# Kernel optimization log

Measured on AMD Instinct MI355X. Metric: run time of the kernel, lower is better.

## Reference

```python
import jax, jax.numpy as jnp
import numpy as np

EPS = 1e-5  # torch LayerNorm default

def _ln(x, w, b):
    mu = jnp.mean(x, axis=-1, keepdims=True)
    var = jnp.mean((x - mu) ** 2, axis=-1, keepdims=True)
    return (x - mu) * jax.lax.rsqrt(var + EPS) * w + b

def setup_inputs() -> dict:
    B, C, P, D = 256, 256, 256, 256  # broadcasting in final add requires B==P==C
    key = jax.random.key(0)
    ks = jax.random.split(key, 10)
    d_rsqrt = D ** -0.5
    return {
        "x": jax.random.normal(ks[0], (B, C), dtype=jnp.float32),
        "prev_cell_out": jax.random.normal(ks[1], (P, D), dtype=jnp.float32),
        "feature_emb_weight": jax.random.uniform(ks[2], (C, D), minval=-d_rsqrt, maxval=d_rsqrt),
        "feature_emb_bias": jax.random.uniform(ks[3], (1, C, D), minval=-d_rsqrt, maxval=d_rsqrt),
        "ln_emb_w": jnp.ones((D,), jnp.float32), "ln_emb_b": jnp.zeros((D,), jnp.float32),
        "ln_col_w": jnp.ones((D,), jnp.float32), "ln_col_b": jnp.zeros((D,), jnp.float32),
        "ln_prompt_w": jnp.ones((D,), jnp.float32), "ln_prompt_b": jnp.zeros((D,), jnp.float32),
        "dense_imp_w": jax.random.normal(ks[4], (D, 2 * D)) * (2 * D) ** -0.5,  # torch Linear weight [out,in]
        "dense_imp_b": jnp.zeros((D,), jnp.float32),
        "emb_column": jax.random.normal(ks[5], (C, D)) * 0.01,
        "emb_prompt": jax.random.normal(ks[6], (P, D)) * 0.01,
        "expand_weight": jax.random.normal(ks[7], (P, 1)),  # dense_expand.weight [n_prompts, 1]
        "expand_bias": jax.random.normal(ks[8], (P,)) * 0.01,
    }

def reference(x, prev_cell_out, feature_emb_weight, feature_emb_bias,
              ln_emb_w, ln_emb_b, ln_col_w, ln_col_b, ln_prompt_w, ln_prompt_b,
              dense_imp_w, dense_imp_b, emb_column, emb_prompt,
              expand_weight, expand_bias):
    # addcmul: bias + x[...,None] * weight -> [B, C, D]
    x_emb = _ln(jax.nn.relu(feature_emb_bias + x[..., None] * feature_emb_weight), ln_emb_w, ln_emb_b)
    # prompt path (unbatched): [P, 2D] -> [P, D]
    xp_in = jnp.concatenate([_ln(emb_prompt, ln_prompt_w, ln_prompt_b), prev_cell_out], axis=-1)
    x_prompt = xp_in @ dense_imp_w.T + dense_imp_b + emb_prompt
    x_col = _ln(emb_column, ln_col_w, ln_col_b)  # [C, D]
    mask = jax.nn.softmax(x_prompt @ x_col.T, axis=-1)  # [P, C]
    # einsum 'pc,bcd->bpd'
    x_out = jnp.einsum('pc,bcd->bpd', mask, x_emb)
    # 'pc,bcd,pa->bpd' with a==1 is the same contraction scaled per-prompt by expand_weight[p,0]
    x_out = x_out * (1.0 + expand_weight[:, 0])[None, :, None]
    # 'pc,p->pc' then unsqueeze(0).unsqueeze(-1): [1, P, C, 1]; broadcasts [B,P,D] -> [1,B,P,D]
    bias_term = (mask * expand_bias[:, None])[None, :, :, None]
    return x_out + bias_term  # [1, B, P, D] (B==P==C)
```

## Files before the change

### kernel.cpp

```cpp
#include <hip/hip_runtime.h>
#include <cstdint>

typedef _Float16 half8 __attribute__((ext_vector_type(8)));
typedef float f32x4 __attribute__((ext_vector_type(4)));

#define LN_EPS 1e-5f

__device__ __forceinline__ void gl2lds16(const void* g, void* l) {
  __builtin_amdgcn_global_load_lds((const __attribute__((address_space(1))) uint32_t*)g,
                                   (__attribute__((address_space(3))) uint32_t*)l, 16, 0, 0);
}

__global__ __launch_bounds__(256) void k_ln_rows(
    const float* __restrict__ emb_prompt, const float* __restrict__ lnp_w, const float* __restrict__ lnp_b,
    const float* __restrict__ emb_column, const float* __restrict__ lnc_w, const float* __restrict__ lnc_b,
    float* __restrict__ out_prompt, float* __restrict__ out_col)
{
  int row = blockIdx.x * 4 + (threadIdx.x >> 6);
  int lane = threadIdx.x & 63;
  const float *src, *wp, *bp; float* dst; int r;
  if (row < 256) { src = emb_prompt; wp = lnp_w; bp = lnp_b; dst = out_prompt; r = row; }
  else           { src = emb_column; wp = lnc_w; bp = lnc_b; dst = out_col;    r = row - 256; }
  float4 v = ((const float4*)src)[r * 64 + lane];
  float s1 = v.x + v.y + v.z + v.w;
  float s2 = v.x*v.x + v.y*v.y + v.z*v.z + v.w*v.w;
  #pragma unroll
  for (int o = 32; o > 0; o >>= 1) { s1 += __shfl_xor(s1, o); s2 += __shfl_xor(s2, o); }
  float mu  = s1 * (1.0f/256.0f);
  float var = s2 * (1.0f/256.0f) - mu*mu;
  float rs  = rsqrtf(var + LN_EPS);
  float4 w4 = ((const float4*)wp)[lane];
  float4 b4 = ((const float4*)bp)[lane];
  float4 y;
  y.x = (v.x-mu)*rs*w4.x + b4.x;
  y.y = (v.y-mu)*rs*w4.y + b4.y;
  y.z = (v.z-mu)*rs*w4.z + b4.z;
  y.w = (v.w-mu)*rs*w4.w + b4.w;
  ((float4*)dst)[r * 64 + lane] = y;
}

__global__ __launch_bounds__(256) void k_xprompt(
    const float* __restrict__ ln_prompt, const float* __restrict__ prev,
    const float* __restrict__ W, const float* __restrict__ bias,
    const float* __restrict__ emb_prompt, float* __restrict__ xprompt)
{
  __shared__ float xp[4][512];
  int t = threadIdx.x;
  int pb = blockIdx.x * 4;
  #pragma unroll
  for (int r = 0; r < 4; ++r) {
    xp[r][t]       = ln_prompt[(pb+r)*256 + t];
    xp[r][256 + t] = prev[(pb+r)*256 + t];
  }
  __syncthreads();
  float acc[4] = {0.f, 0.f, 0.f, 0.f};
  const float4* W4 = (const float4*)(W + (size_t)t * 512);
  for (int k4 = 0; k4 < 128; ++k4) {
    float4 wv = W4[k4];
    #pragma unroll
    for (int r = 0; r < 4; ++r) {
      float4 xq = ((const float4*)xp[r])[k4];
      acc[r] += wv.x*xq.x + wv.y*xq.y + wv.z*xq.z + wv.w*xq.w;
    }
  }
  float bb = bias[t];
  #pragma unroll
  for (int r = 0; r < 4; ++r)
    xprompt[(pb+r)*256 + t] = acc[r] + bb + emb_prompt[(pb+r)*256 + t];
}

__global__ __launch_bounds__(256) void k_mask(
    const float* __restrict__ xprompt, const float* __restrict__ xcol,
    float* __restrict__ mask_f32, _Float16* __restrict__ mask_f16)
{
  __shared__ float xp[4][256];
  __shared__ float4 wred[4];
  __shared__ float4 wred2[4];
  int t = threadIdx.x, w = t >> 6, lane = t & 63;
  int pb = blockIdx.x * 4;
  #pragma unroll
  for (int r = 0; r < 4; ++r) xp[r][t] = xprompt[(pb+r)*256 + t];
  __syncthreads();
  float sc[4] = {0.f, 0.f, 0.f, 0.f};
  const float4* c4 = (const float4*)(xcol + (size_t)t * 256);
  for (int d4 = 0; d4 < 64; ++d4) {
    float4 cv = c4[d4];
    #pragma unroll
    for (int r = 0; r < 4; ++r) {
      float4 xq = ((const float4*)xp[r])[d4];
      sc[r] += cv.x*xq.x + cv.y*xq.y + cv.z*xq.z + cv.w*xq.w;
    }
  }
  float m[4] = {sc[0], sc[1], sc[2], sc[3]};
  #pragma unroll
  for (int o = 32; o > 0; o >>= 1) {
    #pragma unroll
    for (int r = 0; r < 4; ++r) m[r] = fmaxf(m[r], __shfl_xor(m[r], o));
  }
  if (lane == 0) wred[w] = make_float4(m[0], m[1], m[2], m[3]);
  __syncthreads();
  float4 a0 = wred[0], a1 = wred[1], a2 = wred[2], a3 = wred[3];
  float M[4] = { fmaxf(fmaxf(a0.x,a1.x), fmaxf(a2.x,a3.x)),
                 fmaxf(fmaxf(a0.y,a1.y), fmaxf(a2.y,a3.y)),
                 fmaxf(fmaxf(a0.z,a1.z), fmaxf(a2.z,a3.z)),
                 fmaxf(fmaxf(a0.w,a1.w), fmaxf(a2.w,a3.w)) };
  float e[4], s[4];
  #pragma unroll
  for (int r = 0; r < 4; ++r) { e[r] = expf(sc[r] - M[r]); s[r] = e[r]; }
  #pragma unroll
  for (int o = 32; o > 0; o >>= 1) {
    #pragma unroll
    for (int r = 0; r < 4; ++r) s[r] += __shfl_xor(s[r], o);
  }
  if (lane == 0) wred2[w] = make_float4(s[0], s[1], s[2], s[3]);
  __syncthreads();
  float4 b0 = wred2[0], b1 = wred2[1], b2 = wred2[2], b3 = wred2[3];
  float S[4] = { b0.x+b1.x+b2.x+b3.x, b0.y+b1.y+b2.y+b3.y,
                 b0.z+b1.z+b2.z+b3.z, b0.w+b1.w+b2.w+b3.w };
  #pragma unroll
  for (int r = 0; r < 4; ++r) {
    float mv = e[r] / S[r];
    mask_f32[(pb+r)*256 + t] = mv;
    mask_f16[(pb+r)*256 + t] = (_Float16)mv;
  }
}

__global__ __launch_bounds__(256) void k_xemb(
    const float* __restrict__ x, const float* __restrict__ few, const float* __restrict__ feb,
    const float* __restrict__ lnw, const float* __restrict__ lnb, _Float16* __restrict__ emb)
{
  __shared__ float ldsv[8][256];
  __shared__ float stat_mu[8], stat_rs[8];
  int t = threadIdx.x, w = t >> 6, lane = t & 63;
  int b = blockIdx.x >> 5, cg = blockIdx.x & 31;
  float v[8];
  #pragma unroll
  for (int cl = 0; cl < 8; ++cl) {
    int c = cg*8 + cl;
    float xv = x[b*256 + c];
    float val = feb[c*256 + t] + xv * few[c*256 + t];
    v[cl] = fmaxf(val, 0.f);
    ldsv[cl][t] = v[cl];
  }
  __syncthreads();
  #pragma unroll
  for (int j = 0; j < 2; ++j) {
    int cl = w*2 + j;
    float4 a = ((const float4*)ldsv[cl])[lane];
    float s1 = a.x + a.y + a.z + a.w;
    float s2 = a.x*a.x + a.y*a.y + a.z*a.z + a.w*a.w;
    #pragma unroll
    for (int o = 32; o > 0; o >>= 1) { s1 += __shfl_xor(s1, o); s2 += __shfl_xor(s2, o); }
    if (lane == 0) {
      float mu  = s1 * (1.0f/256.0f);
      float var = s2 * (1.0f/256.0f) - mu*mu;
      stat_mu[cl] = mu;
      stat_rs[cl] = rsqrtf(var + LN_EPS);
    }
  }
  __syncthreads();
  float lw = lnw[t], lb = lnb[t];
  half8 h;
  #pragma unroll
  for (int cl = 0; cl < 8; ++cl)
    h[cl] = (_Float16)((v[cl] - stat_mu[cl]) * stat_rs[cl] * lw + lb);
  ((uint4*)emb)[(size_t)cg*65536 + (size_t)b*256 + t] = *(const uint4*)&h;
}

__global__ __launch_bounds__(256) void k_gemm(
    const _Float16* __restrict__ Bmat,
    const _Float16* __restrict__ Amask,
    const float* __restrict__ mask_f32,
    const float* __restrict__ ew, const float* __restrict__ eb,
    float* __restrict__ out)
{
  __shared__ __align__(16) _Float16 As[128 * 72];
  __shared__ __align__(16) _Float16 Bs[8 * 128 * 8];
  int t = threadIdx.x, w = t >> 6, lane = t & 63;
  int lm = lane & 15, quad = lane >> 4;
  int wm = (w & 1) * 64, wn = (w >> 1) * 64;
  int p0 = blockIdx.x * 128;
  int n0 = blockIdx.y * 128;

  f32x4 acc[4][4];
  #pragma unroll
  for (int i = 0; i < 4; ++i)
    #pragma unroll
    for (int j = 0; j < 4; ++j)
      acc[i][j] = (f32x4){0.f, 0.f, 0.f, 0.f};

  for (int kb = 0; kb < 4; ++kb) {
    int k0 = kb * 64;
    if (kb) __syncthreads();
    #pragma unroll
    for (int i = 0; i < 4; ++i) {
      int u = i*256 + t;
      int chi = u >> 7, np = u & 127;
      gl2lds16(Bmat + (size_t)(kb*8 + chi)*524288 + (size_t)(n0 + np)*8, Bs + (size_t)u*8);
    }
    uint4 av[4];
    #pragma unroll
    for (int i = 0; i < 4; ++i) {
      int u = i*256 + t;
      int m = u >> 3, k8 = u & 7;
      av[i] = *(const uint4*)(Amask + (size_t)(p0 + m)*256 + k0 + k8*8);
    }
    #pragma unroll
    for (int i = 0; i < 4; ++i) {
      int u = i*256 + t;
      int m = u >> 3, k8 = u & 7;
      *(uint4*)(As + m*72 + k8*8) = av[i];
    }
    __syncthreads();
    #pragma unroll
    for (int ks = 0; ks < 2; ++ks) {
      half8 af[4], bf[4];
      #pragma unroll
      for (int mt = 0; mt < 4; ++mt)
        af[mt] = *(const half8*)(As + (wm + mt*16 + lm)*72 + ks*32 + quad*8);
      #pragma unroll
      for (int nt = 0; nt < 4; ++nt)
        bf[nt] = *(const half8*)(Bs + ((ks*4 + quad)*128 + wn + nt*16 + lm)*8);
      #pragma unroll
      for (int mt = 0; mt < 4; ++mt)
        #pragma unroll
        for (int nt = 0; nt < 4; ++nt)
          acc[mt][nt] = __builtin_amdgcn_mfma_f32_16x16x32_f16(af[mt], bf[nt], acc[mt][nt], 0, 0, 0);
    }
  }

  int b = n0 >> 8;
  float ebv = eb[b];
  #pragma unroll
  for (int mt = 0; mt < 4; ++mt) {
    float sp[4], tb[4];
    #pragma unroll
    for (int r = 0; r < 4; ++r) {
      int p = p0 + wm + mt*16 + quad*4 + r;
      sp[r] = 1.0f + ew[p];
      tb[r] = mask_f32[b*256 + p] * ebv;
    }
    #pragma unroll
    for (int nt = 0; nt < 4; ++nt) {
      int d = (n0 & 255) + wn + nt*16 + lm;
      #pragma unroll
      for (int r = 0; r < 4; ++r) {
        int p = p0 + wm + mt*16 + quad*4 + r;
        out[((size_t)b << 16) + ((size_t)p << 8) + d] = acc[mt][nt][r] * sp[r] + tb[r];
      }
    }
  }
}

extern "C" void kernel_launch(void* const* d_in, const int* in_sizes, int n_in,
                              void* d_out, int out_size, void* d_ws, size_t ws_size,
                              hipStream_t stream) {
  const float* x        = (const float*)d_in[0];
  const float* prev     = (const float*)d_in[1];
  const float* few      = (const float*)d_in[2];
  const float* feb      = (const float*)d_in[3];
  const float* ln_emb_w = (const float*)d_in[4];
  const float* ln_emb_b = (const float*)d_in[5];
  const float* ln_col_w = (const float*)d_in[6];
  const float* ln_col_b = (const float*)d_in[7];
  const float* ln_pr_w  = (const float*)d_in[8];
  const float* ln_pr_b  = (const float*)d_in[9];
  const float* dimp_w   = (const float*)d_in[10];
  const float* dimp_b   = (const float*)d_in[11];
  const float* emb_col  = (const float*)d_in[12];
  const float* emb_pr   = (const float*)d_in[13];
  const float* ew       = (const float*)d_in[14];
  const float* eb       = (const float*)d_in[15];
  float* out = (float*)d_out;

  char* wsb = (char*)d_ws;
  _Float16* ws_emb    = (_Float16*)(wsb);
  float*    ws_mask   = (float*)(wsb + 33554432);
  _Float16* ws_mask_h = (_Float16*)(wsb + 33816576);
  float*    ws_lnp    = (float*)(wsb + 33947648);
  float*    ws_xcol   = (float*)(wsb + 34209792);
  float*    ws_xp     = (float*)(wsb + 34471936);

  k_ln_rows<<<dim3(128), dim3(256), 0, stream>>>(emb_pr, ln_pr_w, ln_pr_b,
                                                 emb_col, ln_col_w, ln_col_b,
                                                 ws_lnp, ws_xcol);
  k_xprompt<<<dim3(64), dim3(256), 0, stream>>>(ws_lnp, prev, dimp_w, dimp_b, emb_pr, ws_xp);
  k_mask<<<dim3(64), dim3(256), 0, stream>>>(ws_xp, ws_xcol, ws_mask, ws_mask_h);
  k_xemb<<<dim3(8192), dim3(256), 0, stream>>>(x, few, feb, ln_emb_w, ln_emb_b, ws_emb);
  k_gemm<<<dim3(2, 512), dim3(256), 0, stream>>>(ws_emb, ws_mask_h, ws_mask, ew, eb, out);
}
```

Before: 182.0 us.

## Fuse prompt/mask pipeline and x_emb into one kernel; stream A from global in GEMM

Measured after the change: 243.7 us. 33.9% more time.

```diff
diff --git a/kernel.cpp b/kernel.cpp
--- a/kernel.cpp
+++ b/kernel.cpp
@@ -11,171 +11,220 @@
                                    (__attribute__((address_space(3))) uint32_t*)l, 16, 0, 0);
 }
 
-__global__ __launch_bounds__(256) void k_ln_rows(
-    const float* __restrict__ emb_prompt, const float* __restrict__ lnp_w, const float* __restrict__ lnp_b,
-    const float* __restrict__ emb_column, const float* __restrict__ lnc_w, const float* __restrict__ lnc_b,
-    float* __restrict__ out_prompt, float* __restrict__ out_col)
+__device__ __forceinline__ float dot4(float4 a, float4 b) {
+  return a.x*b.x + a.y*b.y + a.z*b.z + a.w*b.w;
+}
+
+__global__ __launch_bounds__(256) void k_fused(
+    const float* __restrict__ x, const float* __restrict__ few, const float* __restrict__ feb,
+    const float* __restrict__ ln_emb_w, const float* __restrict__ ln_emb_b,
+    const float* __restrict__ emb_pr, const float* __restrict__ lnp_w, const float* __restrict__ lnp_b,
+    const float* __restrict__ prev, const float* __restrict__ W, const float* __restrict__ Wb,
+    const float* __restrict__ emb_col, const float* __restrict__ lnc_w, const float* __restrict__ lnc_b,
+    float* __restrict__ mask_f32, _Float16* __restrict__ mask_f16, _Float16* __restrict__ emb)
 {
-  int row = blockIdx.x * 4 + (threadIdx.x >> 6);
-  int lane = threadIdx.x & 63;
-  const float *src, *wp, *bp; float* dst; int r;
-  if (row < 256) { src = emb_prompt; wp = lnp_w; bp = lnp_b; dst = out_prompt; r = row; }
-  else           { src = emb_column; wp = lnc_w; bp = lnc_b; dst = out_col;    r = row - 256; }
-  float4 v = ((const float4*)src)[r * 64 + lane];
-  float s1 = v.x + v.y + v.z + v.w;
-  float s2 = v.x*v.x + v.y*v.y + v.z*v.z + v.w*v.w;
-  #pragma unroll
-  for (int o = 32; o > 0; o >>= 1) { s1 += __shfl_xor(s1, o); s2 += __shfl_xor(s2, o); }
-  float mu  = s1 * (1.0f/256.0f);
-  float var = s2 * (1.0f/256.0f) - mu*mu;
-  float rs  = rsqrtf(var + LN_EPS);
-  float4 w4 = ((const float4*)wp)[lane];
-  float4 b4 = ((const float4*)bp)[lane];
-  float4 y;
-  y.x = (v.x-mu)*rs*w4.x + b4.x;
-  y.y = (v.y-mu)*rs*w4.y + b4.y;
-  y.z = (v.z-mu)*rs*w4.z + b4.z;
-  y.w = (v.w-mu)*rs*w4.w + b4.w;
-  ((float4*)dst)[r * 64 + lane] = y;
-}
-
-__global__ __launch_bounds__(256) void k_xprompt(
-    const float* __restrict__ ln_prompt, const float* __restrict__ prev,
-    const float* __restrict__ W, const float* __restrict__ bias,
-    const float* __restrict__ emb_prompt, float* __restrict__ xprompt)
-{
-  __shared__ float xp[4][512];
-  int t = threadIdx.x;
-  int pb = blockIdx.x * 4;
-  #pragma unroll
-  for (int r = 0; r < 4; ++r) {
-    xp[r][t]       = ln_prompt[(pb+r)*256 + t];
-    xp[r][256 + t] = prev[(pb+r)*256 + t];
+  __shared__ __align__(16) union SMem {
+    struct {
+      float xin[4][512];
+      float xq[4][256];
+      float cmu[256], crs[256];
+      float sc[4][256];
+      float4 wr1[4], wr2[4];
+    } m;
+    struct {
+      float v[32][256];
+      float mu[32], rs[32];
+    } e;
+  } sm;
+
+  int t = threadIdx.x, w = t >> 6, lane = t & 63;
+
+  if (blockIdx.x < 64) {
+    int pb = blockIdx.x * 4;
+    {
+      int p = pb + w;
+      float4 v = ((const float4*)emb_pr)[p * 64 + lane];
+      float s1 = v.x + v.y + v.z + v.w;
+      float s2 = v.x*v.x + v.y*v.y + v.z*v.z + v.w*v.w;
+      #pragma unroll
+      for (int o = 32; o > 0; o >>= 1) { s1 += __shfl_xor(s1, o); s2 += __shfl_xor(s2, o); }
+      float mu = s1 * (1.0f/256.0f);
+      float var = s2 * (1.0f/256.0f) - mu*mu;
+      float rs = rsqrtf(var + LN_EPS);
+      float4 w4 = ((const float4*)lnp_w)[lane];
+      float4 b4 = ((const float4*)lnp_b)[lane];
+      float4 y;
+      y.x = (v.x-mu)*rs*w4.x + b4.x;  y.y = (v.y-mu)*rs*w4.y + b4.y;
+      y.z = (v.z-mu)*rs*w4.z + b4.z;  y.w = (v.w-mu)*rs*w4.w + b4.w;
+      ((float4*)sm.m.xin[w])[lane] = y;
+      ((float4*)sm.m.xin[w])[64 + lane] = ((const float4*)prev)[p * 64 + lane];
+    }
+    for (int i = 0; i < 64; ++i) {
+      int c = w * 64 + i;
+      float4 v = ((const float4*)emb_col)[c * 64 + lane];
+      float s1 = v.x + v.y + v.z + v.w;
+      float s2 = v.x*v.x + v.y*v.y + v.z*v.z + v.w*v.w;
+      #pragma unroll
+      for (int o = 32; o > 0; o >>= 1) { s1 += __shfl_xor(s1, o); s2 += __shfl_xor(s2, o); }
+      if (lane == 0) {
+        float mu = s1 * (1.0f/256.0f);
+        float var = s2 * (1.0f/256.0f) - mu*mu;
+        sm.m.cmu[c] = mu;
+        sm.m.crs[c] = rsqrtf(var + LN_EPS);
+      }
+    }
+    __syncthreads();
+    {
+      float4 xa[4], xb[4];
+      #pragma unroll
+      for (int r = 0; r < 4; ++r) {
+        xa[r] = ((const float4*)sm.m.xin[r])[lane];
+        xb[r] = ((const float4*)sm.m.xin[r])[64 + lane];
+      }
+      for (int i = 0; i < 64; ++i) {
+        int d = w * 64 + i;
+        float4 wa = ((const float4*)W)[d * 128 + lane];
+        float4 wc = ((const float4*)W)[d * 128 + 64 + lane];
+        float a0 = dot4(wa, xa[0]) + dot4(wc, xb[0]);
+        float a1 = dot4(wa, xa[1]) + dot4(wc, xb[1]);
+        float a2 = dot4(wa, xa[2]) + dot4(wc, xb[2]);
+        float a3 = dot4(wa, xa[3]) + dot4(wc, xb[3]);
+        #pragma unroll
+        for (int o = 32; o > 0; o >>= 1) {
+          a0 += __shfl_xor(a0, o); a1 += __shfl_xor(a1, o);
+          a2 += __shfl_xor(a2, o); a3 += __shfl_xor(a3, o);
+        }
+        if (lane == 0) {
+          float bb = Wb[d];
+          sm.m.xq[0][d] = a0 + bb + emb_pr[(pb+0)*256 + d];
+          sm.m.xq[1][d] = a1 + bb + emb_pr[(pb+1)*256 + d];
+          sm.m.xq[2][d] = a2 + bb + emb_pr[(pb+2)*256 + d];
+          sm.m.xq[3][d] = a3 + bb + emb_pr[(pb+3)*256 + d];
+        }
+      }
+    }
+    __syncthreads();
+    {
+      float4 lw4 = ((const float4*)lnc_w)[lane];
+      float4 lb4 = ((const float4*)lnc_b)[lane];
+      float4 xr[4];
+      #pragma unroll
+      for (int r = 0; r < 4; ++r) xr[r] = ((const float4*)sm.m.xq[r])[lane];
+      for (int i = 0; i < 64; ++i) {
+        int c = w * 64 + i;
+        float4 v = ((const float4*)emb_col)[c * 64 + lane];
+        float mu = sm.m.cmu[c], rs = sm.m.crs[c];
+        float4 nc;
+        nc.x = (v.x-mu)*rs*lw4.x + lb4.x;  nc.y = (v.y-mu)*rs*lw4.y + lb4.y;
+        nc.z = (v.z-mu)*rs*lw4.z + lb4.z;  nc.w = (v.w-mu)*rs*lw4.w + lb4.w;
+        float a0 = dot4(nc, xr[0]), a1 = dot4(nc, xr[1]);
+        float a2 = dot4(nc, xr[2]), a3 = dot4(nc, xr[3]);
+        #pragma unroll
+        for (int o = 32; o > 0; o >>= 1) {
+          a0 += __shfl_xor(a0, o); a1 += __shfl_xor(a1, o);
+          a2 += __shfl_xor(a2, o); a3 += __shfl_xor(a3, o);
+        }
+        if (lane == 0) {
+          sm.m.sc[0][c] = a0; sm.m.sc[1][c] = a1;
+          sm.m.sc[2][c] = a2; sm.m.sc[3][c] = a3;
+        }
+      }
+    }
+    __syncthreads();
+    {
+      float val[4];
+      #pragma unroll
+      for (int r = 0; r < 4; ++r) val[r] = sm.m.sc[r][t];
+      float m0[4] = {val[0], val[1], val[2], val[3]};
+      #pragma unroll
+      for (int o = 32; o > 0; o >>= 1)
+        #pragma unroll
+        for (int r = 0; r < 4; ++r) m0[r] = fmaxf(m0[r], __shfl_xor(m0[r], o));
+      if (lane == 0) sm.m.wr1[w] = make_float4(m0[0], m0[1], m0[2], m0[3]);
+      __syncthreads();
+      float4 a0 = sm.m.wr1[0], a1 = sm.m.wr1[1], a2 = sm.m.wr1[2], a3 = sm.m.wr1[3];
+      float M[4] = { fmaxf(fmaxf(a0.x,a1.x), fmaxf(a2.x,a3.x)),
+                     fmaxf(fmaxf(a0.y,a1.y), fmaxf(a2.y,a3.y)),
+                     fmaxf(fmaxf(a0.z,a1.z), fmaxf(a2.z,a3.z)),
+                     fmaxf(fmaxf(a0.w,a1.w), fmaxf(a2.w,a3.w)) };
+      float e[4], s[4];
+      #pragma unroll
+      for (int r = 0; r < 4; ++r) { e[r] = expf(val[r] - M[r]); s[r] = e[r]; }
+      #pragma unroll
+      for (int o = 32; o > 0; o >>= 1)
+        #pragma unroll
+        for (int r = 0; r < 4; ++r) s[r] += __shfl_xor(s[r], o);
+      if (lane == 0) sm.m.wr2[w] = make_float4(s[0], s[1], s[2], s[3]);
+      __syncthreads();
+      float4 b0 = sm.m.wr2[0], b1 = sm.m.wr2[1], b2 = sm.m.wr2[2], b3 = sm.m.wr2[3];
+      float S[4] = { b0.x+b1.x+b2.x+b3.x, b0.y+b1.y+b2.y+b3.y,
+                     b0.z+b1.z+b2.z+b3.z, b0.w+b1.w+b2.w+b3.w };
+      #pragma unroll
+      for (int r = 0; r < 4; ++r) {
+        float mv = e[r] / S[r];
+        mask_f32[(pb+r)*256 + t] = mv;
+        mask_f16[(pb+r)*256 + t] = (_Float16)mv;
+      }
+    }
+  } else {
+    int bid = blockIdx.x - 64;
+    int cg = bid & 31, bg = bid >> 5;
+    float fw[8], fb[8];
+    #pragma unroll
+    for (int cl = 0; cl < 8; ++cl) {
+      int c = cg*8 + cl;
+      fw[cl] = few[c*256 + t];
+      fb[cl] = feb[c*256 + t];
+    }
+    float v[4][8];
+    #pragma unroll
+    for (int j = 0; j < 4; ++j) {
+      int b = bg*4 + j;
+      #pragma unroll
+      for (int cl = 0; cl < 8; ++cl) {
+        float xv = x[b*256 + cg*8 + cl];
+        v[j][cl] = fmaxf(fb[cl] + xv*fw[cl], 0.f);
+        sm.e.v[j*8 + cl][t] = v[j][cl];
+      }
+    }
+    __syncthreads();
+    #pragma unroll
+    for (int jj = 0; jj < 8; ++jj) {
+      int row = w*8 + jj;
+      float4 a = ((const float4*)sm.e.v[row])[lane];
+      float s1 = a.x + a.y + a.z + a.w;
+      float s2 = a.x*a.x + a.y*a.y + a.z*a.z + a.w*a.w;
+      #pragma unroll
+      for (int o = 32; o > 0; o >>= 1) { s1 += __shfl_xor(s1, o); s2 += __shfl_xor(s2, o); }
+      if (lane == 0) {
+        float mu = s1 * (1.0f/256.0f);
+        float var = s2 * (1.0f/256.0f) - mu*mu;
+        sm.e.mu[row] = mu;
+        sm.e.rs[row] = rsqrtf(var + LN_EPS);
+      }
+    }
+    __syncthreads();
+    float lw = ln_emb_w[t], lb = ln_emb_b[t];
+    #pragma unroll
+    for (int j = 0; j < 4; ++j) {
+      half8 h;
+      #pragma unroll
+      for (int cl = 0; cl < 8; ++cl) {
+        int row = j*8 + cl;
+        h[cl] = (_Float16)((v[j][cl] - sm.e.mu[row]) * sm.e.rs[row] * lw + lb);
+      }
+      ((uint4*)emb)[(size_t)cg*65536 + (size_t)(bg*4 + j)*256 + t] = *(const uint4*)&h;
+    }
   }
-  __syncthreads();
-  float acc[4] = {0.f, 0.f, 0.f, 0.f};
-  const float4* W4 = (const float4*)(W + (size_t)t * 512);
-  for (int k4 = 0; k4 < 128; ++k4) {
-    float4 wv = W4[k4];
-    #pragma unroll
-    for (int r = 0; r < 4; ++r) {
-      float4 xq = ((const float4*)xp[r])[k4];
-      acc[r] += wv.x*xq.x + wv.y*xq.y + wv.z*xq.z + wv.w*xq.w;
-    }
-  }
-  float bb = bias[t];
-  #pragma unroll
-  for (int r = 0; r < 4; ++r)
-    xprompt[(pb+r)*256 + t] = acc[r] + bb + emb_prompt[(pb+r)*256 + t];
-}
-
-__global__ __launch_bounds__(256) void k_mask(
-    const float* __restrict__ xprompt, const float* __restrict__ xcol,
-    float* __restrict__ mask_f32, _Float16* __restrict__ mask_f16)
-{
-  __shared__ float xp[4][256];
-  __shared__ float4 wred[4];
-  __shared__ float4 wred2[4];
-  int t = threadIdx.x, w = t >> 6, lane = t & 63;
-  int pb = blockIdx.x * 4;
-  #pragma unroll
-  for (int r = 0; r < 4; ++r) xp[r][t] = xprompt[(pb+r)*256 + t];
-  __syncthreads();
-  float sc[4] = {0.f, 0.f, 0.f, 0.f};
-  const float4* c4 = (const float4*)(xcol + (size_t)t * 256);
-  for (int d4 = 0; d4 < 64; ++d4) {
-    float4 cv = c4[d4];
-    #pragma unroll
-    for (int r = 0; r < 4; ++r) {
-      float4 xq = ((const float4*)xp[r])[d4];
-      sc[r] += cv.x*xq.x + cv.y*xq.y + cv.z*xq.z + cv.w*xq.w;
-    }
-  }
-  float m[4] = {sc[0], sc[1], sc[2], sc[3]};
-  #pragma unroll
-  for (int o = 32; o > 0; o >>= 1) {
-    #pragma unroll
-    for (int r = 0; r < 4; ++r) m[r] = fmaxf(m[r], __shfl_xor(m[r], o));
-  }
-  if (lane == 0) wred[w] = make_float4(m[0], m[1], m[2], m[3]);
-  __syncthreads();
-  float4 a0 = wred[0], a1 = wred[1], a2 = wred[2], a3 = wred[3];
-  float M[4] = { fmaxf(fmaxf(a0.x,a1.x), fmaxf(a2.x,a3.x)),
-                 fmaxf(fmaxf(a0.y,a1.y), fmaxf(a2.y,a3.y)),
-                 fmaxf(fmaxf(a0.z,a1.z), fmaxf(a2.z,a3.z)),
-                 fmaxf(fmaxf(a0.w,a1.w), fmaxf(a2.w,a3.w)) };
-  float e[4], s[4];
-  #pragma unroll
-  for (int r = 0; r < 4; ++r) { e[r] = expf(sc[r] - M[r]); s[r] = e[r]; }
-  #pragma unroll
-  for (int o = 32; o > 0; o >>= 1) {
-    #pragma unroll
-    for (int r = 0; r < 4; ++r) s[r] += __shfl_xor(s[r], o);
-  }
-  if (lane == 0) wred2[w] = make_float4(s[0], s[1], s[2], s[3]);
-  __syncthreads();
-  float4 b0 = wred2[0], b1 = wred2[1], b2 = wred2[2], b3 = wred2[3];
-  float S[4] = { b0.x+b1.x+b2.x+b3.x, b0.y+b1.y+b2.y+b3.y,
-                 b0.z+b1.z+b2.z+b3.z, b0.w+b1.w+b2.w+b3.w };
-  #pragma unroll
-  for (int r = 0; r < 4; ++r) {
-    float mv = e[r] / S[r];
-    mask_f32[(pb+r)*256 + t] = mv;
-    mask_f16[(pb+r)*256 + t] = (_Float16)mv;
-  }
-}
-
-__global__ __launch_bounds__(256) void k_xemb(
-    const float* __restrict__ x, const float* __restrict__ few, const float* __restrict__ feb,
-    const float* __restrict__ lnw, const float* __restrict__ lnb, _Float16* __restrict__ emb)
-{
-  __shared__ float ldsv[8][256];
-  __shared__ float stat_mu[8], stat_rs[8];
-  int t = threadIdx.x, w = t >> 6, lane = t & 63;
-  int b = blockIdx.x >> 5, cg = blockIdx.x & 31;
-  float v[8];
-  #pragma unroll
-  for (int cl = 0; cl < 8; ++cl) {
-    int c = cg*8 + cl;
-    float xv = x[b*256 + c];
-    float val = feb[c*256 + t] + xv * few[c*256 + t];
-    v[cl] = fmaxf(val, 0.f);
-    ldsv[cl][t] = v[cl];
-  }
-  __syncthreads();
-  #pragma unroll
-  for (int j = 0; j < 2; ++j) {
-    int cl = w*2 + j;
-    float4 a = ((const float4*)ldsv[cl])[lane];
-    float s1 = a.x + a.y + a.z + a.w;
-    float s2 = a.x*a.x + a.y*a.y + a.z*a.z + a.w*a.w;
-    #pragma unroll
-    for (int o = 32; o > 0; o >>= 1) { s1 += __shfl_xor(s1, o); s2 += __shfl_xor(s2, o); }
-    if (lane == 0) {
-      float mu  = s1 * (1.0f/256.0f);
-      float var = s2 * (1.0f/256.0f) - mu*mu;
-      stat_mu[cl] = mu;
-      stat_rs[cl] = rsqrtf(var + LN_EPS);
-    }
-  }
-  __syncthreads();
-  float lw = lnw[t], lb = lnb[t];
-  half8 h;
-  #pragma unroll
-  for (int cl = 0; cl < 8; ++cl)
-    h[cl] = (_Float16)((v[cl] - stat_mu[cl]) * stat_rs[cl] * lw + lb);
-  ((uint4*)emb)[(size_t)cg*65536 + (size_t)b*256 + t] = *(const uint4*)&h;
 }
 
 __global__ __launch_bounds__(256) void k_gemm(
-    const _Float16* __restrict__ Bmat,
-    const _Float16* __restrict__ Amask,
+    const _Float16* __restrict__ Bmat, const _Float16* __restrict__ Amask,
     const float* __restrict__ mask_f32,
     const float* __restrict__ ew, const float* __restrict__ eb,
     float* __restrict__ out)
 {
-  __shared__ __align__(16) _Float16 As[128 * 72];
-  __shared__ __align__(16) _Float16 Bs[8 * 128 * 8];
+  __shared__ __align__(16) _Float16 Bs[16 * 128 * 8];
   int t = threadIdx.x, w = t >> 6, lane = t & 63;
   int lm = lane & 15, quad = lane >> 4;
   int wm = (w & 1) * 64, wn = (w >> 1) * 64;
@@ -189,35 +238,23 @@
     for (int j = 0; j < 4; ++j)
       acc[i][j] = (f32x4){0.f, 0.f, 0.f, 0.f};
 
-  for (int kb = 0; kb < 4; ++kb) {
-    int k0 = kb * 64;
+  #pragma unroll
+  for (int kb = 0; kb < 2; ++kb) {
     if (kb) __syncthreads();
     #pragma unroll
-    for (int i = 0; i < 4; ++i) {
+    for (int i = 0; i < 8; ++i) {
       int u = i*256 + t;
       int chi = u >> 7, np = u & 127;
-      gl2lds16(Bmat + (size_t)(kb*8 + chi)*524288 + (size_t)(n0 + np)*8, Bs + (size_t)u*8);
-    }
-    uint4 av[4];
-    #pragma unroll
-    for (int i = 0; i < 4; ++i) {
-      int u = i*256 + t;
-      int m = u >> 3, k8 = u & 7;
-      av[i] = *(const uint4*)(Amask + (size_t)(p0 + m)*256 + k0 + k8*8);
-    }
-    #pragma unroll
-    for (int i = 0; i < 4; ++i) {
-      int u = i*256 + t;
-      int m = u >> 3, k8 = u & 7;
-      *(uint4*)(As + m*72 + k8*8) = av[i];
-    }
-    __syncthreads();
-    #pragma unroll
-    for (int ks = 0; ks < 2; ++ks) {
+      gl2lds16(Bmat + (size_t)(kb*16 + chi)*524288 + (size_t)(n0 + np)*8, Bs + (size_t)u*8);
+    }
+    __syncthreads();
+    #pragma unroll
+    for (int ks = 0; ks < 4; ++ks) {
+      int k0 = kb*128 + ks*32 + quad*8;
       half8 af[4], bf[4];
       #pragma unroll
       for (int mt = 0; mt < 4; ++mt)
-        af[mt] = *(const half8*)(As + (wm + mt*16 + lm)*72 + ks*32 + quad*8);
+        af[mt] = *(const half8*)(Amask + (size_t)(p0 + wm + mt*16 + lm)*256 + k0);
       #pragma unroll
       for (int nt = 0; nt < 4; ++nt)
         bf[nt] = *(const half8*)(Bs + ((ks*4 + quad)*128 + wn + nt*16 + lm)*8);
@@ -277,15 +314,11 @@
   _Float16* ws_emb    = (_Float16*)(wsb);
   float*    ws_mask   = (float*)(wsb + 33554432);
   _Float16* ws_mask_h = (_Float16*)(wsb + 33816576);
-  float*    ws_lnp    = (float*)(wsb + 33947648);
-  float*    ws_xcol   = (float*)(wsb + 34209792);
-  float*    ws_xp     = (float*)(wsb + 34471936);
-
-  k_ln_rows<<<dim3(128), dim3(256), 0, stream>>>(emb_pr, ln_pr_w, ln_pr_b,
-                                                 emb_col, ln_col_w, ln_col_b,
-                                                 ws_lnp, ws_xcol);
-  k_xprompt<<<dim3(64), dim3(256), 0, stream>>>(ws_lnp, prev, dimp_w, dimp_b, emb_pr, ws_xp);
-  k_mask<<<dim3(64), dim3(256), 0, stream>>>(ws_xp, ws_xcol, ws_mask, ws_mask_h);
-  k_xemb<<<dim3(8192), dim3(256), 0, stream>>>(x, few, feb, ln_emb_w, ln_emb_b, ws_emb);
+
+  k_fused<<<dim3(64 + 2048), dim3(256), 0, stream>>>(
+      x, few, feb, ln_emb_w, ln_emb_b,
+      emb_pr, ln_pr_w, ln_pr_b, prev, dimp_w, dimp_b,
+      emb_col, ln_col_w, ln_col_b,
+      ws_mask, ws_mask_h, ws_emb);
   k_gemm<<<dim3(2, 512), dim3(256), 0, stream>>>(ws_emb, ws_mask_h, ws_mask, ew, eb, out);
 }
```
